# Kernel tuning notes

Hardware: AMD Instinct MI355X
Metric: run time of the kernel (lower is better)

The kernel has to match this reference:

```python
import jax, jax.numpy as jnp
import numpy as np

B, S, D, H = 8, 2048, 1024, 1024

def setup_inputs() -> dict:
    key = jax.random.key(0)
    ks = jax.random.split(key, 7)
    s = 1.0 / np.sqrt(D)  # torch Linear default init scale (uniform bound)
    x = jax.random.normal(ks[0], (B, S, D), dtype=jnp.float32)
    Wq = jax.random.uniform(ks[1], (D, H), jnp.float32, -s, s)
    bq = jax.random.uniform(ks[2], (H,), jnp.float32, -s, s)
    Wk = jax.random.uniform(ks[3], (D, H), jnp.float32, -s, s)
    bk = jax.random.uniform(ks[4], (H,), jnp.float32, -s, s)
    Wv = jax.random.uniform(ks[5], (D, H), jnp.float32, -s, s)
    bv = jax.random.uniform(ks[6], (H,), jnp.float32, -s, s)
    return {"x": x, "Wq": Wq, "bq": bq, "Wk": Wk, "bk": bk, "Wv": Wv, "bv": bv}

def reference(x, Wq, bq, Wk, bk, Wv, bv):
    scale = jnp.asarray(H ** 0.5, x.dtype)
    q = jnp.einsum('bsd,dh->bsh', x, Wq) + bq
    k = jnp.einsum('bsd,dh->bsh', x, Wk) + bk
    v = jnp.einsum('bsd,dh->bsh', x, Wv) + bv
    scores = jnp.einsum('bqh,bkh->bqk', q, k) / scale  # [B,S,S]
    probs = jax.nn.softmax(scores, axis=-1)
    return jnp.einsum('bqk,bkh->bqh', probs, v)
```

## Files before the change

### kernel.cpp

```cpp
#include <hip/hip_runtime.h>
#include <hip/hip_bf16.h>
#include <stdint.h>

using bf16 = __hip_bfloat16;
typedef __bf16 bf16x8 __attribute__((ext_vector_type(8)));
typedef float f32x4 __attribute__((ext_vector_type(4)));
typedef unsigned short u16x8 __attribute__((ext_vector_type(8)));

#define GLOAD_LDS16(gp, lp)                                                    \
  __builtin_amdgcn_global_load_lds(                                           \
      (const __attribute__((address_space(1))) void*)(gp),                     \
      (__attribute__((address_space(3))) void*)(lp), 16, 0, 0)

#define WAITCNT_VM(N) asm volatile("s_waitcnt vmcnt(" #N ")" ::: "memory")
#define WAITCNT_LGKM0() asm volatile("s_waitcnt lgkmcnt(0)" ::: "memory")

__device__ inline void store_out(bf16* p, float v)  { *p = __float2bfloat16(v); }
__device__ inline void store_out(float* p, float v) { *p = v; }

template <typename OUT_T, int BIAS_AXIS>
__global__ __launch_bounds__(512, 2) void gemm256(
    const bf16* __restrict__ A, const bf16* __restrict__ Bt,
    const float* __restrict__ bias0, const float* __restrict__ bias1,
    OUT_T* __restrict__ out0, OUT_T* __restrict__ out1, int Nsplit,
    int K, int lda, int ldb, int ldc,
    long long sA, long long sB, long long sC, float alpha)
{
    __shared__ __align__(16) bf16 lds[4 * 16384];

    const int z = blockIdx.z;
    A  += (long long)z * sA;
    Bt += (long long)z * sB;
    out0 += (long long)z * sC;
    if (out1) out1 += (long long)z * sC;

    const int bm = blockIdx.x * 256;
    const int bn = blockIdx.y * 256;
    const int t = threadIdx.x, lane = t & 63, w = t >> 6;
    const int wm = w >> 2, wn = w & 3;
    const int fr = lane & 15, c16 = lane >> 4;

    const bf16* gsrc[4];
    int lbase[4];
    #pragma unroll
    for (int c = 0; c < 4; ++c) {
        const int idx  = w * 128 + (c & 1) * 64 + lane;
        const int slot = idx & 7;
        const int r    = ((idx >> 3) << 1) | (idx & 1);
        const int cc   = (slot ^ (r & 7)) >> 1;
        if (c < 2) {
            gsrc[c]  = A + (long long)(bm + r) * lda + cc * 8;
            lbase[c] = w * 1024 + c * 512;
        } else {
            gsrc[c]  = Bt + (long long)(bn + r) * ldb + cc * 8;
            lbase[c] = 8192 + w * 1024 + (c - 2) * 512;
        }
    }

    const int sw   = ((fr & 7) ^ (c16 << 1)) * 8;
    const int offA = (wm * 64 + (fr >> 1)) * 64 + sw;
    const int offB = 8192 + (wn * 32 + (fr >> 1)) * 64 + sw;

    const int nk = K >> 5;

    auto STAGE = [&](int jt) {
        const int buf = (jt & 3) * 16384;
        #pragma unroll
        for (int c = 0; c < 4; ++c)
            GLOAD_LDS16(gsrc[c] + jt * 32, &lds[buf + lbase[c]]);
    };

    STAGE(0); STAGE(1); STAGE(2);
    WAITCNT_VM(8);
    __builtin_amdgcn_s_barrier();

    f32x4 acc[8][4] = {};

    for (int j = 0; j < nk; ++j) {
        const int buf = (j & 3) * 16384;
        if (j + 3 < nk) STAGE(j + 3);

        bf16x8 af[8], bfv[4];
        #pragma unroll
        for (int m = 0; m < 8; ++m)
            af[m] = *reinterpret_cast<const bf16x8*>(&lds[buf + offA + m * 512]);
        #pragma unroll
        for (int n = 0; n < 4; ++n)
            bfv[n] = *reinterpret_cast<const bf16x8*>(&lds[buf + offB + n * 512]);

        WAITCNT_LGKM0();
        __builtin_amdgcn_sched_barrier(0);

        #pragma unroll
        for (int m = 0; m < 8; ++m)
            #pragma unroll
            for (int n = 0; n < 4; ++n)
                acc[m][n] = __builtin_amdgcn_mfma_f32_16x16x32_bf16(
                    af[m], bfv[n], acc[m][n], 0, 0, 0);

        if (j + 3 < nk)      { WAITCNT_VM(8); }
        else if (j + 2 < nk) { WAITCNT_VM(4); }
        else if (j + 1 < nk) { WAITCNT_VM(0); }
        __builtin_amdgcn_s_barrier();
    }

    const int colbase = bn + wn * 64 + fr;
    const int rowbase = bm + wm * 128 + c16 * 4;
    #pragma unroll
    for (int n = 0; n < 4; ++n) {
        const int gc = colbase + n * 16;
        const bool seg0 = gc < Nsplit;
        OUT_T* op = seg0 ? out0 : out1;
        const int col = seg0 ? gc : gc - Nsplit;
        float bcol = 0.0f;
        if (BIAS_AXIS == 0) {
            const float* bp = seg0 ? bias0 : bias1;
            if (bp) bcol = bp[col];
        }
        #pragma unroll
        for (int m = 0; m < 8; ++m) {
            #pragma unroll
            for (int jj = 0; jj < 4; ++jj) {
                const int row = rowbase + m * 16 + jj;
                float v = acc[m][n][jj] * alpha;
                if (BIAS_AXIS == 0) v += bcol;
                else if (bias0)     v += bias0[row];
                store_out(&op[(long long)row * ldc + col], v);
            }
        }
    }
}

__global__ __launch_bounds__(256) void f32_to_bf16(
    const float* __restrict__ in, bf16* __restrict__ out, long long n)
{
    long long i = ((long long)blockIdx.x * 256 + threadIdx.x) * 4;
    const long long stride = (long long)gridDim.x * 256 * 4;
    for (; i < n; i += stride) {
        float4 v = *reinterpret_cast<const float4*>(in + i);
        unsigned ux = __float_as_uint(v.x), uy = __float_as_uint(v.y);
        unsigned uz = __float_as_uint(v.z), uw = __float_as_uint(v.w);
        ushort4 o;
        o.x = (unsigned short)((ux + 0x7fffu + ((ux >> 16) & 1u)) >> 16);
        o.y = (unsigned short)((uy + 0x7fffu + ((uy >> 16) & 1u)) >> 16);
        o.z = (unsigned short)((uz + 0x7fffu + ((uz >> 16) & 1u)) >> 16);
        o.w = (unsigned short)((uw + 0x7fffu + ((uw >> 16) & 1u)) >> 16);
        *reinterpret_cast<ushort4*>(out + i) = o;
    }
}

__global__ void transpose_f32_bf16(const float* __restrict__ in,
                                   bf16* __restrict__ out, int R, int C)
{
    __shared__ float tile[32][33];
    const int c0 = blockIdx.x * 32, r0 = blockIdx.y * 32;
    const int tx = threadIdx.x, ty = threadIdx.y;
    #pragma unroll
    for (int i = ty; i < 32; i += 8)
        tile[i][tx] = in[(long long)(r0 + i) * C + (c0 + tx)];
    __syncthreads();
    #pragma unroll
    for (int i = ty; i < 32; i += 8)
        out[(long long)(c0 + i) * R + (r0 + tx)] = __float2bfloat16(tile[tx][i]);
}

__global__ __launch_bounds__(256) void softmax_rows(bf16* __restrict__ Sbuf, int cols)
{
    __shared__ float red[8];
    bf16* p = Sbuf + (long long)blockIdx.x * cols;
    const int t = threadIdx.x;

    u16x8 v = *reinterpret_cast<const u16x8*>(p + t * 8);
    float f[8];
    #pragma unroll
    for (int i = 0; i < 8; ++i)
        f[i] = __uint_as_float((unsigned)v[i] << 16);

    float m = -3.0e38f;
    #pragma unroll
    for (int i = 0; i < 8; ++i) m = fmaxf(m, f[i]);
    #pragma unroll
    for (int o = 32; o; o >>= 1) m = fmaxf(m, __shfl_xor(m, o));
    if ((t & 63) == 0) red[t >> 6] = m;
    __syncthreads();
    m = fmaxf(fmaxf(red[0], red[1]), fmaxf(red[2], red[3]));

    float s = 0.0f;
    #pragma unroll
    for (int i = 0; i < 8; ++i) { f[i] = __expf(f[i] - m); s += f[i]; }
    #pragma unroll
    for (int o = 32; o; o >>= 1) s += __shfl_xor(s, o);
    __syncthreads();
    if ((t & 63) == 0) red[4 + (t >> 6)] = s;
    __syncthreads();
    s = (red[4] + red[5]) + (red[6] + red[7]);
    const float inv = 1.0f / s;

    u16x8 o16;
    #pragma unroll
    for (int i = 0; i < 8; ++i) {
        unsigned u = __float_as_uint(f[i] * inv);
        o16[i] = (unsigned short)((u + 0x7fffu + ((u >> 16) & 1u)) >> 16);
    }
    *reinterpret_cast<u16x8*>(p + t * 8) = o16;
}

extern "C" void kernel_launch(void* const* d_in, const int* in_sizes, int n_in,
                              void* d_out, int out_size, void* d_ws, size_t ws_size,
                              hipStream_t stream)
{
    const int B = 8, S = 2048, D = 1024, H = 1024;
    const float* x  = (const float*)d_in[0];
    const float* Wq = (const float*)d_in[1];
    const float* bq = (const float*)d_in[2];
    const float* Wk = (const float*)d_in[3];
    const float* bk = (const float*)d_in[4];
    const float* Wv = (const float*)d_in[5];
    const float* bv = (const float*)d_in[6];
    float* out = (float*)d_out;

    const size_t nQKV = (size_t)B * S * H;
    const size_t nW   = (size_t)D * H;
    const long long sSH = (long long)S * H;
    const long long sSS = (long long)S * S;

    dim3 tb(32, 8), g256(256), g512(512);
    const float inv_scale = 1.0f / 32.0f;

    bf16* xb   = (bf16*)d_ws;
    bf16* Q    = xb  + nQKV;
    bf16* Kb   = Q   + nQKV;
    bf16* Vt   = Kb  + nQKV;
    bf16* WtQK = Vt  + nQKV;
    bf16* Wtv  = WtQK + 2 * nW;
    bf16* Sc   = Wtv + nW;

    const size_t tierA = (4 * nQKV + 3 * nW + (size_t)B * S * S) * 2;
    const size_t tierB = (4 * nQKV + 3 * nW + (size_t)S * S) * 2;
    const bool bigA = ws_size >= tierA;
    if (ws_size < tierB) return;

    f32_to_bf16<<<dim3(2048), g256, 0, stream>>>(x, xb, (long long)nQKV);
    transpose_f32_bf16<<<dim3(H / 32, D / 32), tb, 0, stream>>>(Wq, WtQK, D, H);
    transpose_f32_bf16<<<dim3(H / 32, D / 32), tb, 0, stream>>>(Wk, WtQK + nW, D, H);
    transpose_f32_bf16<<<dim3(H / 32, D / 32), tb, 0, stream>>>(Wv, Wtv, D, H);

    gemm256<bf16, 0><<<dim3(B * S / 256, 2 * H / 256, 1), g512, 0, stream>>>(
        xb, WtQK, bq, bk, Q, Kb, H, D, D, D, H, 0, 0, 0, 1.0f);

    gemm256<bf16, 1><<<dim3(H / 256, B * S / 256, 1), g512, 0, stream>>>(
        Wtv, xb, bv, nullptr, Vt, nullptr, 1 << 30, D, D, D, B * S, 0, 0, 0, 1.0f);

    if (bigA) {
        gemm256<bf16, 0><<<dim3(S / 256, S / 256, B), g512, 0, stream>>>(
            Q, Kb, nullptr, nullptr, Sc, nullptr, 1 << 30, H, H, H, S,
            sSH, sSH, sSS, inv_scale);
        softmax_rows<<<dim3(B * S), g256, 0, stream>>>(Sc, S);
        gemm256<float, 0><<<dim3(S / 256, H / 256, B), g512, 0, stream>>>(
            Sc, Vt, nullptr, nullptr, out, nullptr, 1 << 30, S, S, B * S, H,
            sSS, (long long)S, sSH, 1.0f);
    } else {
        for (int b = 0; b < B; ++b) {
            gemm256<bf16, 0><<<dim3(S / 256, S / 256, 1), g512, 0, stream>>>(
                Q + (size_t)b * sSH, Kb + (size_t)b * sSH, nullptr, nullptr,
                Sc, nullptr, 1 << 30, H, H, H, S, 0, 0, 0, inv_scale);
            softmax_rows<<<dim3(S), g256, 0, stream>>>(Sc, S);
            gemm256<float, 0><<<dim3(S / 256, H / 256, 1), g512, 0, stream>>>(
                Sc, Vt + (size_t)b * S, nullptr, nullptr,
                out + (size_t)b * sSH, nullptr, 1 << 30, S, S, B * S, H,
                0, 0, 0, 1.0f);
        }
    }
}
```

Before: 346.8 us.

## Split GEMM k-step into two half-phases interleaving LDS reads, prefetch and MFMA

Each k-iteration of the 256-tile GEMM main loop is split into two phases. Each phase issues half of the A-fragment LDS reads and half of the global-to-LDS prefetch, then runs 16 MFMAs at raised wave priority (s_setprio). Extra workgroup barriers keep the waves in step. The goal is to interleave memory issue with matrix-core work across the waves of a CU, a ping-pong style schedule. The cost is more barriers per iteration, which may add stall time.

```diff
diff --git a/kernel.cpp b/kernel.cpp
--- a/kernel.cpp
+++ b/kernel.cpp
@@ -63,14 +63,15 @@
 
     const int nk = K >> 5;
 
-    auto STAGE = [&](int jt) {
+    auto STAGE2 = [&](int jt, int h) {
         const int buf = (jt & 3) * 16384;
-        #pragma unroll
-        for (int c = 0; c < 4; ++c)
-            GLOAD_LDS16(gsrc[c] + jt * 32, &lds[buf + lbase[c]]);
+        GLOAD_LDS16(gsrc[2 * h]     + jt * 32, &lds[buf + lbase[2 * h]]);
+        GLOAD_LDS16(gsrc[2 * h + 1] + jt * 32, &lds[buf + lbase[2 * h + 1]]);
     };
 
-    STAGE(0); STAGE(1); STAGE(2);
+    STAGE2(0, 0); STAGE2(0, 1);
+    STAGE2(1, 0); STAGE2(1, 1);
+    STAGE2(2, 0); STAGE2(2, 1);
     WAITCNT_VM(8);
     __builtin_amdgcn_s_barrier();
 
@@ -78,25 +79,49 @@
 
     for (int j = 0; j < nk; ++j) {
         const int buf = (j & 3) * 16384;
-        if (j + 3 < nk) STAGE(j + 3);
-
-        bf16x8 af[8], bfv[4];
-        #pragma unroll
-        for (int m = 0; m < 8; ++m)
+        const bool pref = (j + 3 < nk);
+
+        bf16x8 af[4], bfv[4], af2[4];
+        #pragma unroll
+        for (int m = 0; m < 4; ++m)
             af[m] = *reinterpret_cast<const bf16x8*>(&lds[buf + offA + m * 512]);
         #pragma unroll
         for (int n = 0; n < 4; ++n)
             bfv[n] = *reinterpret_cast<const bf16x8*>(&lds[buf + offB + n * 512]);
-
+        if (pref) STAGE2(j + 3, 0);
+
+        __builtin_amdgcn_s_barrier();
         WAITCNT_LGKM0();
         __builtin_amdgcn_sched_barrier(0);
-
-        #pragma unroll
-        for (int m = 0; m < 8; ++m)
+        __builtin_amdgcn_s_setprio(1);
+        #pragma unroll
+        for (int m = 0; m < 4; ++m)
             #pragma unroll
             for (int n = 0; n < 4; ++n)
                 acc[m][n] = __builtin_amdgcn_mfma_f32_16x16x32_bf16(
                     af[m], bfv[n], acc[m][n], 0, 0, 0);
+        __builtin_amdgcn_s_setprio(0);
+        __builtin_amdgcn_sched_barrier(0);
+        __builtin_amdgcn_s_barrier();
+
+        #pragma unroll
+        for (int m = 0; m < 4; ++m)
+            af2[m] = *reinterpret_cast<const bf16x8*>(
+                &lds[buf + offA + (m + 4) * 512]);
+        if (pref) STAGE2(j + 3, 1);
+
+        __builtin_amdgcn_s_barrier();
+        WAITCNT_LGKM0();
+        __builtin_amdgcn_sched_barrier(0);
+        __builtin_amdgcn_s_setprio(1);
+        #pragma unroll
+        for (int m = 0; m < 4; ++m)
+            #pragma unroll
+            for (int n = 0; n < 4; ++n)
+                acc[m + 4][n] = __builtin_amdgcn_mfma_f32_16x16x32_bf16(
+                    af2[m], bfv[n], acc[m + 4][n], 0, 0, 0);
+        __builtin_amdgcn_s_setprio(0);
+        __builtin_amdgcn_sched_barrier(0);
 
         if (j + 3 < nk)      { WAITCNT_VM(8); }
         else if (j + 2 < nk) { WAITCNT_VM(4); }
```

New measurement: 353.6 us. No clear change (+2.0%).
